# Kernel optimization log

Measured on AMD Instinct MI355X. Metric: run time of the kernel, lower is better.

## Reference

```python
import jax, jax.numpy as jnp
import numpy as np
from functools import reduce
from jax.scipy.linalg import block_diag

M = 3          # ancilla / layered-matrix qubits
NQ = 4         # QNN qubits
L = 8          # num_qnn_layers
NOUT = 4       # number of QNN blocks
DIM_A = 2 ** M   # 8
DIM_Q = 2 ** NQ  # 16
BATCH = 131072


def _ry(t):
    # RY rotation: [[cos(t/2), -sin(t/2)], [sin(t/2), cos(t/2)]]
    c = jnp.cos(t * 0.5)
    s = jnp.sin(t * 0.5)
    return jnp.stack([jnp.stack([c, -s]), jnp.stack([s, c])])


def _cnot_full(n, c, t):
    # dense CNOT on n qubits (control c, target t), built once as a constant
    dim = 2 ** n
    P = np.zeros((dim, dim), np.float32)
    for i in range(dim):
        bits = [(i >> (n - 1 - k)) & 1 for k in range(n)]
        if bits[c] == 1:
            bits[t] ^= 1
        j = sum(b << (n - 1 - k) for k, b in enumerate(bits))
        P[j, i] = 1.0
    return jnp.asarray(P)

# entangling layer: CNOT(0,1) then CNOT(1,2) then CNOT(2,3) -> matrix product in reverse
_ENT = reduce(lambda acc, g: g @ acc, [_cnot_full(NQ, q, q + 1) for q in range(NQ - 1)], jnp.eye(DIM_Q))


def _build_qnn(thetas):  # thetas: (L, NQ) -> 16x16 unitary
    U = jnp.eye(DIM_Q)
    for l in range(L):
        rys = reduce(jnp.kron, [_ry(thetas[l, q]) for q in range(NQ)])
        U = _ENT @ (rys @ U)
    return U


def _layered_product_matrix(alpha):
    # hierarchical tree of RY blocks: layer l has 2^l rotations, block-diagonal,
    # kron'd with identity on the remaining qubits; product over layers.
    U = jnp.eye(DIM_A)
    idx = 0
    for l in range(M):
        nb = 2 ** l
        bd = block_diag(*[_ry(alpha[idx + b]) for b in range(nb)])
        idx += nb
        U = jnp.kron(bd, jnp.eye(2 ** (M - l - 1))) @ U
    return U


def setup_inputs() -> dict:
    key = jax.random.key(0)
    k1, k2, k3 = jax.random.split(key, 3)
    x = jax.random.uniform(k1, (BATCH, 4), dtype=jnp.float32)
    alpha = jax.random.uniform(k2, (2 ** M - 1,), dtype=jnp.float32) * 6.28
    qnn_thetas = jax.random.uniform(k3, (NOUT, L * NQ), dtype=jnp.float32) * 6.28
    return {"x": x, "alpha": alpha, "qnn_thetas": qnn_thetas}


def reference(x, alpha, qnn_thetas):
    b = x.shape[0]
    ang = x * (np.pi / 0.5)  # (b, 4)
    c = jnp.cos(ang * 0.5)
    s = jnp.sin(ang * 0.5)
    # per-qubit RY|0> amplitudes -> encoding state = kron of the four 2-vectors
    v = [jnp.stack([c[:, q], s[:, q]], axis=1) for q in range(NQ)]
    enc = jnp.einsum('bi,bj,bk,bl->bijkl', *v).reshape(b, DIM_Q)  # (b, 16)
    ent0 = _layered_product_matrix(alpha)[:, 0]                    # (8,) = U_ent |0>
    inter = ent0[None, :, None] * enc[:, None, :]                  # (b, 8, 16) = kron state
    qnn = [_build_qnn(qnn_thetas[j].reshape(L, NQ)) for j in range(NOUT)]
    blocks = jnp.stack(qnn + [jnp.eye(DIM_Q)] * (DIM_A - NOUT))    # (8, 16, 16) block-diagonal
    fin = jnp.einsum('kij,bkj->bki', blocks, inter)                # (b, 8, 16)
    # measure Z on qubits 3,4,5 (first three QNN qubits)
    p = (fin * fin).reshape(b, DIM_A, 2, 2, 2, 2)
    z = jnp.array([1.0, -1.0], dtype=x.dtype)
    e3 = jnp.einsum('bkijlm,i->b', p, z)
    e4 = jnp.einsum('bkijlm,j->b', p, z)
    e5 = jnp.einsum('bkijlm,l->b', p, z)
    return (jnp.stack([e3, e4, e5], axis=1) + 1.0) * 0.5           # (b, 3)
```

## Files before the change

kernel.cpp:

```cpp
#include <hip/hip_runtime.h>

#define NLAY 8
#define TPB 256
#define SPT 2

__global__ __launch_bounds__(TPB) void qnn_fused(const float4* __restrict__ x,
                                                 const float* __restrict__ alpha,
                                                 const float* __restrict__ thetas,
                                                 float* __restrict__ out,
                                                 int batch, int nthreads) {
    __shared__ float2 csT[128];
    __shared__ float2 csA[8];
    __shared__ float  U[4][16][20];
    __shared__ float  w4s;
    __shared__ float  Af[3][16][16];
    __shared__ float  Mf[3][10][12];

    const int tid = threadIdx.x;
    const int gid = blockIdx.x * TPB + tid;

    float4 xv[SPT];
    #pragma unroll
    for (int s = 0; s < SPT; ++s) {
        const int b = gid + s * nthreads;
        xv[s] = x[(b < batch) ? b : 0];
    }

    if (tid < 128) {
        const float t = thetas[tid] * 0.5f;
        csT[tid] = make_float2(cosf(t), sinf(t));
    } else if (tid < 135) {
        const float t = alpha[tid - 128] * 0.5f;
        csA[tid - 128] = make_float2(cosf(t), sinf(t));
    }
    __syncthreads();

    if (tid < 64) {
        float e[8];
        #pragma unroll
        for (int i = 0; i < 8; ++i) e[i] = (i == 0) ? 1.0f : 0.0f;
        int idx = 0;
        #pragma unroll
        for (int l = 0; l < 3; ++l) {
            const int p = 2 - l, pb = 1 << p;
            #pragma unroll
            for (int i0 = 0; i0 < 8; ++i0) {
                if (i0 & pb) continue;
                const int i1 = i0 | pb;
                const float2 cs = csA[idx + (i0 >> (p + 1))];
                const float a0 = e[i0], a1 = e[i1];
                e[i0] = cs.x * a0 - cs.y * a1;
                e[i1] = cs.y * a0 + cs.x * a1;
            }
            idx += (1 << l);
        }
        if (tid == 0)
            w4s = e[4]*e[4] + e[5]*e[5] + e[6]*e[6] + e[7]*e[7];

        const int k = tid >> 4, col = tid & 15;
        float st[16];
        #pragma unroll
        for (int i = 0; i < 16; ++i) st[i] = (i == col) ? 1.0f : 0.0f;
        #pragma unroll 1
        for (int l = 0; l < NLAY; ++l) {
            #pragma unroll
            for (int q = 0; q < 4; ++q) {
                const float2 cs = csT[k * 32 + l * 4 + q];
                const int pb = 1 << (3 - q);
                #pragma unroll
                for (int i0 = 0; i0 < 16; ++i0) {
                    if (i0 & pb) continue;
                    const int i1 = i0 | pb;
                    const float a0 = st[i0], a1 = st[i1];
                    st[i0] = cs.x * a0 - cs.y * a1;
                    st[i1] = cs.y * a0 + cs.x * a1;
                }
            }
            #pragma unroll
            for (int q = 0; q < 3; ++q) {
                const int cb = 1 << (3 - q), tb = 1 << (2 - q);
                #pragma unroll
                for (int i = 0; i < 16; ++i) {
                    if ((i & cb) && !(i & tb)) {
                        const int j = i | tb;
                        const float tmp = st[i]; st[i] = st[j]; st[j] = tmp;
                    }
                }
            }
        }
        const float sw = e[k];
        float4* dst = (float4*)&U[k][col][0];
        dst[0] = make_float4(st[0]*sw,  st[1]*sw,  st[2]*sw,  st[3]*sw);
        dst[1] = make_float4(st[4]*sw,  st[5]*sw,  st[6]*sw,  st[7]*sw);
        dst[2] = make_float4(st[8]*sw,  st[9]*sw,  st[10]*sw, st[11]*sw);
        dst[3] = make_float4(st[12]*sw, st[13]*sw, st[14]*sw, st[15]*sw);
    }
    __syncthreads();

    if (tid < 136) {
        int r = tid, t = 0;
        while (r >= 16 - t) { r -= 16 - t; ++t; }
        const int u = t + r;

        float gs[8] = {0,0,0,0,0,0,0,0};
        #pragma unroll
        for (int k = 0; k < 4; ++k) {
            const float4* ct = (const float4*)&U[k][t][0];
            const float4* cu = (const float4*)&U[k][u][0];
            const float4 a0 = ct[0], a1 = ct[1], a2 = ct[2], a3 = ct[3];
            const float4 c0 = cu[0], c1 = cu[1], c2 = cu[2], c3 = cu[3];
            gs[0] = fmaf(a0.x, c0.x, gs[0]); gs[0] = fmaf(a0.y, c0.y, gs[0]);
            gs[1] = fmaf(a0.z, c0.z, gs[1]); gs[1] = fmaf(a0.w, c0.w, gs[1]);
            gs[2] = fmaf(a1.x, c1.x, gs[2]); gs[2] = fmaf(a1.y, c1.y, gs[2]);
            gs[3] = fmaf(a1.z, c1.z, gs[3]); gs[3] = fmaf(a1.w, c1.w, gs[3]);
            gs[4] = fmaf(a2.x, c2.x, gs[4]); gs[4] = fmaf(a2.y, c2.y, gs[4]);
            gs[5] = fmaf(a2.z, c2.z, gs[5]); gs[5] = fmaf(a2.w, c2.w, gs[5]);
            gs[6] = fmaf(a3.x, c3.x, gs[6]); gs[6] = fmaf(a3.y, c3.y, gs[6]);
            gs[7] = fmaf(a3.z, c3.z, gs[7]); gs[7] = fmaf(a3.w, c3.w, gs[7]);
        }
        float A0 = 0.f, A1 = 0.f, A2 = 0.f;
        #pragma unroll
        for (int c = 0; c < 8; ++c) {
            const float g = gs[c];
            A0 += (c & 4) ? -g : g;
            A1 += (c & 2) ? -g : g;
            A2 += (c & 1) ? -g : g;
        }
        if (t == u) {
            const float w4 = w4s;
            A0 += ((t >> 3) & 1) ? -w4 : w4;
            A1 += ((t >> 2) & 1) ? -w4 : w4;
            A2 += ((t >> 1) & 1) ? -w4 : w4;
        }
        Af[0][t][u] = A0; Af[0][u][t] = A0;
        Af[1][t][u] = A1; Af[1][u][t] = A1;
        Af[2][t][u] = A2; Af[2][u][t] = A2;
    }
    __syncthreads();

    for (int e = tid; e < 360; e += TPB) {
        const int m = e / 120, rr = e - m * 120, p = rr / 12, q = rr - p * 12;
        float v = 0.0f;
        if (q < 10) {
            int i, k, jj, ll;
            if (p < 4)      { i = 0; k = p; }
            else if (p < 7) { i = 1; k = p - 3; }
            else if (p < 9) { i = 2; k = p - 5; }
            else            { i = 3; k = 3; }
            if (q < 4)      { jj = 0; ll = q; }
            else if (q < 7) { jj = 1; ll = q - 3; }
            else if (q < 9) { jj = 2; ll = q - 5; }
            else            { jj = 3; ll = 3; }
            if (i < k && jj < ll)       v = Af[m][4*i+jj][4*k+ll] + Af[m][4*i+ll][4*k+jj];
            else if (i == k && jj < ll) v = Af[m][4*i+jj][4*i+ll];
            else if (i < k && jj == ll) v = Af[m][4*i+jj][4*k+jj];
            else                        v = 0.5f * Af[m][4*i+jj][4*i+jj];
        }
        Mf[m][p][q] = v;
    }
    __syncthreads();

    float G01[SPT][10], G23[SPT][10], acc[SPT][3];
    #pragma unroll
    for (int s = 0; s < SPT; ++s) {
        float c0, s0, c1, s1, c2, s2, c3, s3;
        sincospif(xv[s].x, &s0, &c0);
        sincospif(xv[s].y, &s1, &c1);
        sincospif(xv[s].z, &s2, &c2);
        sincospif(xv[s].w, &s3, &c3);
        float f01[4], f23[4];
        f01[0] = c0 * c1; f01[1] = c0 * s1; f01[2] = s0 * c1; f01[3] = s0 * s1;
        f23[0] = c2 * c3; f23[1] = c2 * s3; f23[2] = s2 * c3; f23[3] = s2 * s3;
        int idx = 0;
        #pragma unroll
        for (int i = 0; i < 4; ++i)
            #pragma unroll
            for (int k = i; k < 4; ++k) { G01[s][idx] = f01[i] * f01[k]; ++idx; }
        idx = 0;
        #pragma unroll
        for (int j = 0; j < 4; ++j)
            #pragma unroll
            for (int l = j; l < 4; ++l) { G23[s][idx] = f23[j] * f23[l]; ++idx; }
        acc[s][0] = 0.5f; acc[s][1] = 0.5f; acc[s][2] = 0.5f;
    }

    #pragma unroll
    for (int p = 0; p < 10; ++p) {
        const float4 m00 = *(const float4*)&Mf[0][p][0];
        const float4 m01 = *(const float4*)&Mf[0][p][4];
        const float4 m02 = *(const float4*)&Mf[0][p][8];
        const float4 m10 = *(const float4*)&Mf[1][p][0];
        const float4 m11 = *(const float4*)&Mf[1][p][4];
        const float4 m12 = *(const float4*)&Mf[1][p][8];
        const float4 m20 = *(const float4*)&Mf[2][p][0];
        const float4 m21 = *(const float4*)&Mf[2][p][4];
        const float4 m22 = *(const float4*)&Mf[2][p][8];
        #pragma unroll
        for (int s = 0; s < SPT; ++s) {
            float z0, z1, z2;
            z0 = m00.x * G23[s][0];
            z1 = m10.x * G23[s][0];
            z2 = m20.x * G23[s][0];
            z0 = fmaf(m00.y, G23[s][1], z0);
            z1 = fmaf(m10.y, G23[s][1], z1);
            z2 = fmaf(m20.y, G23[s][1], z2);
            z0 = fmaf(m00.z, G23[s][2], z0);
            z1 = fmaf(m10.z, G23[s][2], z1);
            z2 = fmaf(m20.z, G23[s][2], z2);
            z0 = fmaf(m00.w, G23[s][3], z0);
            z1 = fmaf(m10.w, G23[s][3], z1);
            z2 = fmaf(m20.w, G23[s][3], z2);
            z0 = fmaf(m01.x, G23[s][4], z0);
            z1 = fmaf(m11.x, G23[s][4], z1);
            z2 = fmaf(m21.x, G23[s][4], z2);
            z0 = fmaf(m01.y, G23[s][5], z0);
            z1 = fmaf(m11.y, G23[s][5], z1);
            z2 = fmaf(m21.y, G23[s][5], z2);
            z0 = fmaf(m01.z, G23[s][6], z0);
            z1 = fmaf(m11.z, G23[s][6], z1);
            z2 = fmaf(m21.z, G23[s][6], z2);
            z0 = fmaf(m01.w, G23[s][7], z0);
            z1 = fmaf(m11.w, G23[s][7], z1);
            z2 = fmaf(m21.w, G23[s][7], z2);
            z0 = fmaf(m02.x, G23[s][8], z0);
            z1 = fmaf(m12.x, G23[s][8], z1);
            z2 = fmaf(m22.x, G23[s][8], z2);
            z0 = fmaf(m02.y, G23[s][9], z0);
            z1 = fmaf(m12.y, G23[s][9], z1);
            z2 = fmaf(m22.y, G23[s][9], z2);
            acc[s][0] = fmaf(G01[s][p], z0, acc[s][0]);
            acc[s][1] = fmaf(G01[s][p], z1, acc[s][1]);
            acc[s][2] = fmaf(G01[s][p], z2, acc[s][2]);
        }
    }

    #pragma unroll
    for (int s = 0; s < SPT; ++s) {
        const int b = gid + s * nthreads;
        if (b < batch) {
            out[b * 3 + 0] = acc[s][0];
            out[b * 3 + 1] = acc[s][1];
            out[b * 3 + 2] = acc[s][2];
        }
    }
}

extern "C" void kernel_launch(void* const* d_in, const int* in_sizes, int n_in,
                              void* d_out, int out_size, void* d_ws, size_t ws_size,
                              hipStream_t stream) {
    const float* x      = (const float*)d_in[0];
    const float* alpha  = (const float*)d_in[1];
    const float* thetas = (const float*)d_in[2];

    const int batch = in_sizes[0] / 4;
    const int blocks = (batch + TPB * SPT - 1) / (TPB * SPT);
    const int nthreads = blocks * TPB;
    qnn_fused<<<blocks, TPB, 0, stream>>>((const float4*)x, alpha, thetas,
                                          (float*)d_out, batch, nthreads);
}
```

Measured before the change: 14.32 us.

## Use packed fp16 dot products for inner contraction and hoist per-sample features

The Mf coefficient table is now stored as packed half2 pairs, and the G23 feature products are converted to half2. The inner 10-term contraction becomes five v_dot2 fp16 operations per output instead of ten fp32 FMAs. The per-sample trig and feature computation moves before the first barrier so it can overlap the matrix-building phase. This halves inner-loop ALU work and LDS reads, at the cost of fp16 rounding error in both the matrix coefficients and the features.

```diff
diff --git a/kernel.cpp b/kernel.cpp
--- a/kernel.cpp
+++ b/kernel.cpp
@@ -1,20 +1,26 @@
 #include <hip/hip_runtime.h>
+
+typedef __fp16 half2_t __attribute__((ext_vector_type(2)));
 
 #define NLAY 8
 #define TPB 256
 #define SPT 2
+
+static __device__ __forceinline__ half2_t bch(int v) {
+    return __builtin_bit_cast(half2_t, v);
+}
 
 __global__ __launch_bounds__(TPB) void qnn_fused(const float4* __restrict__ x,
                                                  const float* __restrict__ alpha,
                                                  const float* __restrict__ thetas,
                                                  float* __restrict__ out,
                                                  int batch, int nthreads) {
-    __shared__ float2 csT[128];
-    __shared__ float2 csA[8];
-    __shared__ float  U[4][16][20];
-    __shared__ float  w4s;
-    __shared__ float  Af[3][16][16];
-    __shared__ float  Mf[3][10][12];
+    __shared__ float2  csT[128];
+    __shared__ float2  csA[8];
+    __shared__ float   U[4][16][20];
+    __shared__ float   w4s;
+    __shared__ float   Af[3][16][16];
+    __shared__ half2_t Mh[3][10][8];
 
     const int tid = threadIdx.x;
     const int gid = blockIdx.x * TPB + tid;
@@ -32,6 +38,35 @@
     } else if (tid < 135) {
         const float t = alpha[tid - 128] * 0.5f;
         csA[tid - 128] = make_float2(cosf(t), sinf(t));
+    }
+
+    float G01[SPT][10], acc[SPT][3];
+    half2_t gh[SPT][5];
+    #pragma unroll
+    for (int s = 0; s < SPT; ++s) {
+        float c0, s0, c1, s1, c2, s2, c3, s3;
+        sincospif(xv[s].x, &s0, &c0);
+        sincospif(xv[s].y, &s1, &c1);
+        sincospif(xv[s].z, &s2, &c2);
+        sincospif(xv[s].w, &s3, &c3);
+        float f01[4], f23[4];
+        f01[0] = c0 * c1; f01[1] = c0 * s1; f01[2] = s0 * c1; f01[3] = s0 * s1;
+        f23[0] = c2 * c3; f23[1] = c2 * s3; f23[2] = s2 * c3; f23[3] = s2 * s3;
+        int idx = 0;
+        #pragma unroll
+        for (int i = 0; i < 4; ++i)
+            #pragma unroll
+            for (int k = i; k < 4; ++k) { G01[s][idx] = f01[i] * f01[k]; ++idx; }
+        float G23[10];
+        idx = 0;
+        #pragma unroll
+        for (int j = 0; j < 4; ++j)
+            #pragma unroll
+            for (int l = j; l < 4; ++l) { G23[idx] = f23[j] * f23[l]; ++idx; }
+        #pragma unroll
+        for (int j = 0; j < 5; ++j)
+            gh[s][j] = __builtin_amdgcn_cvt_pkrtz(G23[2*j], G23[2*j + 1]);
+        acc[s][0] = 0.5f; acc[s][1] = 0.5f; acc[s][2] = 0.5f;
     }
     __syncthreads();
 
@@ -138,96 +173,59 @@
     }
     __syncthreads();
 
-    for (int e = tid; e < 360; e += TPB) {
-        const int m = e / 120, rr = e - m * 120, p = rr / 12, q = rr - p * 12;
-        float v = 0.0f;
-        if (q < 10) {
-            int i, k, jj, ll;
-            if (p < 4)      { i = 0; k = p; }
-            else if (p < 7) { i = 1; k = p - 3; }
-            else if (p < 9) { i = 2; k = p - 5; }
-            else            { i = 3; k = 3; }
+    if (tid < 150) {
+        const int m = tid / 50, rr = tid - m * 50, p = rr / 5, jp = rr - p * 5;
+        int i, k;
+        if (p < 4)      { i = 0; k = p; }
+        else if (p < 7) { i = 1; k = p - 3; }
+        else if (p < 9) { i = 2; k = p - 5; }
+        else            { i = 3; k = 3; }
+        float v[2];
+        #pragma unroll
+        for (int h = 0; h < 2; ++h) {
+            const int q = 2 * jp + h;
+            int jj, ll;
             if (q < 4)      { jj = 0; ll = q; }
             else if (q < 7) { jj = 1; ll = q - 3; }
             else if (q < 9) { jj = 2; ll = q - 5; }
             else            { jj = 3; ll = 3; }
-            if (i < k && jj < ll)       v = Af[m][4*i+jj][4*k+ll] + Af[m][4*i+ll][4*k+jj];
-            else if (i == k && jj < ll) v = Af[m][4*i+jj][4*i+ll];
-            else if (i < k && jj == ll) v = Af[m][4*i+jj][4*k+jj];
-            else                        v = 0.5f * Af[m][4*i+jj][4*i+jj];
-        }
-        Mf[m][p][q] = v;
-    }
-    __syncthreads();
-
-    float G01[SPT][10], G23[SPT][10], acc[SPT][3];
-    #pragma unroll
-    for (int s = 0; s < SPT; ++s) {
-        float c0, s0, c1, s1, c2, s2, c3, s3;
-        sincospif(xv[s].x, &s0, &c0);
-        sincospif(xv[s].y, &s1, &c1);
-        sincospif(xv[s].z, &s2, &c2);
-        sincospif(xv[s].w, &s3, &c3);
-        float f01[4], f23[4];
-        f01[0] = c0 * c1; f01[1] = c0 * s1; f01[2] = s0 * c1; f01[3] = s0 * s1;
-        f23[0] = c2 * c3; f23[1] = c2 * s3; f23[2] = s2 * c3; f23[3] = s2 * s3;
-        int idx = 0;
-        #pragma unroll
-        for (int i = 0; i < 4; ++i)
-            #pragma unroll
-            for (int k = i; k < 4; ++k) { G01[s][idx] = f01[i] * f01[k]; ++idx; }
-        idx = 0;
-        #pragma unroll
-        for (int j = 0; j < 4; ++j)
-            #pragma unroll
-            for (int l = j; l < 4; ++l) { G23[s][idx] = f23[j] * f23[l]; ++idx; }
-        acc[s][0] = 0.5f; acc[s][1] = 0.5f; acc[s][2] = 0.5f;
-    }
+            if (i < k && jj < ll)       v[h] = Af[m][4*i+jj][4*k+ll] + Af[m][4*i+ll][4*k+jj];
+            else if (i == k && jj < ll) v[h] = Af[m][4*i+jj][4*i+ll];
+            else if (i < k && jj == ll) v[h] = Af[m][4*i+jj][4*k+jj];
+            else                        v[h] = 0.5f * Af[m][4*i+jj][4*i+jj];
+        }
+        Mh[m][p][jp] = __builtin_amdgcn_cvt_pkrtz(v[0], v[1]);
+    }
+    __syncthreads();
 
     #pragma unroll
     for (int p = 0; p < 10; ++p) {
-        const float4 m00 = *(const float4*)&Mf[0][p][0];
-        const float4 m01 = *(const float4*)&Mf[0][p][4];
-        const float4 m02 = *(const float4*)&Mf[0][p][8];
-        const float4 m10 = *(const float4*)&Mf[1][p][0];
-        const float4 m11 = *(const float4*)&Mf[1][p][4];
-        const float4 m12 = *(const float4*)&Mf[1][p][8];
-        const float4 m20 = *(const float4*)&Mf[2][p][0];
-        const float4 m21 = *(const float4*)&Mf[2][p][4];
-        const float4 m22 = *(const float4*)&Mf[2][p][8];
+        const int4 i0 = *(const int4*)&Mh[0][p][0];
+        const int  t0 = *(const int*)&Mh[0][p][4];
+        const int4 i1 = *(const int4*)&Mh[1][p][0];
+        const int  t1 = *(const int*)&Mh[1][p][4];
+        const int4 i2 = *(const int4*)&Mh[2][p][0];
+        const int  t2 = *(const int*)&Mh[2][p][4];
+        const half2_t h00 = bch(i0.x), h01 = bch(i0.y), h02 = bch(i0.z), h03 = bch(i0.w), h04 = bch(t0);
+        const half2_t h10 = bch(i1.x), h11 = bch(i1.y), h12 = bch(i1.z), h13 = bch(i1.w), h14 = bch(t1);
+        const half2_t h20 = bch(i2.x), h21 = bch(i2.y), h22 = bch(i2.z), h23 = bch(i2.w), h24 = bch(t2);
         #pragma unroll
         for (int s = 0; s < SPT; ++s) {
-            float z0, z1, z2;
-            z0 = m00.x * G23[s][0];
-            z1 = m10.x * G23[s][0];
-            z2 = m20.x * G23[s][0];
-            z0 = fmaf(m00.y, G23[s][1], z0);
-            z1 = fmaf(m10.y, G23[s][1], z1);
-            z2 = fmaf(m20.y, G23[s][1], z2);
-            z0 = fmaf(m00.z, G23[s][2], z0);
-            z1 = fmaf(m10.z, G23[s][2], z1);
-            z2 = fmaf(m20.z, G23[s][2], z2);
-            z0 = fmaf(m00.w, G23[s][3], z0);
-            z1 = fmaf(m10.w, G23[s][3], z1);
-            z2 = fmaf(m20.w, G23[s][3], z2);
-            z0 = fmaf(m01.x, G23[s][4], z0);
-            z1 = fmaf(m11.x, G23[s][4], z1);
-            z2 = fmaf(m21.x, G23[s][4], z2);
-            z0 = fmaf(m01.y, G23[s][5], z0);
-            z1 = fmaf(m11.y, G23[s][5], z1);
-            z2 = fmaf(m21.y, G23[s][5], z2);
-            z0 = fmaf(m01.z, G23[s][6], z0);
-            z1 = fmaf(m11.z, G23[s][6], z1);
-            z2 = fmaf(m21.z, G23[s][6], z2);
-            z0 = fmaf(m01.w, G23[s][7], z0);
-            z1 = fmaf(m11.w, G23[s][7], z1);
-            z2 = fmaf(m21.w, G23[s][7], z2);
-            z0 = fmaf(m02.x, G23[s][8], z0);
-            z1 = fmaf(m12.x, G23[s][8], z1);
-            z2 = fmaf(m22.x, G23[s][8], z2);
-            z0 = fmaf(m02.y, G23[s][9], z0);
-            z1 = fmaf(m12.y, G23[s][9], z1);
-            z2 = fmaf(m22.y, G23[s][9], z2);
+            float z0 = __builtin_amdgcn_fdot2(h00, gh[s][0], 0.0f, false);
+            float z1 = __builtin_amdgcn_fdot2(h10, gh[s][0], 0.0f, false);
+            float z2 = __builtin_amdgcn_fdot2(h20, gh[s][0], 0.0f, false);
+            z0 = __builtin_amdgcn_fdot2(h01, gh[s][1], z0, false);
+            z1 = __builtin_amdgcn_fdot2(h11, gh[s][1], z1, false);
+            z2 = __builtin_amdgcn_fdot2(h21, gh[s][1], z2, false);
+            z0 = __builtin_amdgcn_fdot2(h02, gh[s][2], z0, false);
+            z1 = __builtin_amdgcn_fdot2(h12, gh[s][2], z1, false);
+            z2 = __builtin_amdgcn_fdot2(h22, gh[s][2], z2, false);
+            z0 = __builtin_amdgcn_fdot2(h03, gh[s][3], z0, false);
+            z1 = __builtin_amdgcn_fdot2(h13, gh[s][3], z1, false);
+            z2 = __builtin_amdgcn_fdot2(h23, gh[s][3], z2, false);
+            z0 = __builtin_amdgcn_fdot2(h04, gh[s][4], z0, false);
+            z1 = __builtin_amdgcn_fdot2(h14, gh[s][4], z1, false);
+            z2 = __builtin_amdgcn_fdot2(h24, gh[s][4], z2, false);
             acc[s][0] = fmaf(G01[s][p], z0, acc[s][0]);
             acc[s][1] = fmaf(G01[s][p], z1, acc[s][1]);
             acc[s][2] = fmaf(G01[s][p], z2, acc[s][2]);
```

After: 12.95 us. -9.5%, faster.
